# Optimization experiments

Measured on AMD Instinct MI355X. Metric: run time of the kernel, lower is better.

The kernel has to match this reference:

```python
import jax, jax.numpy as jnp
import numpy as np

D_MODEL = 1024
NUM_HEADS = 16
D_K = D_MODEL // NUM_HEADS


def setup_inputs() -> dict:
    key = jax.random.key(0)
    ks = jax.random.split(key, 11)
    B, S = 2, 2048
    scale = 1.0 / np.sqrt(D_MODEL)
    inp = {
        "q": jax.random.normal(ks[0], (B, S, D_MODEL), jnp.float32),
        "k": jax.random.normal(ks[1], (B, S, D_MODEL), jnp.float32),
        "v": jax.random.normal(ks[2], (B, S, D_MODEL), jnp.float32),
        "wq_w": jax.random.normal(ks[3], (D_MODEL, D_MODEL), jnp.float32) * scale,
        "wq_b": jnp.zeros((D_MODEL,), jnp.float32),
        "wk_w": jax.random.normal(ks[4], (D_MODEL, D_MODEL), jnp.float32) * scale,
        "wk_b": jnp.zeros((D_MODEL,), jnp.float32),
        "wv_w": jax.random.normal(ks[5], (D_MODEL, D_MODEL), jnp.float32) * scale,
        "wv_b": jnp.zeros((D_MODEL,), jnp.float32),
        "wo_w": jax.random.normal(ks[6], (D_MODEL, D_MODEL), jnp.float32) * scale,
        "wo_b": jnp.zeros((D_MODEL,), jnp.float32),
    }
    return inp


def reference(q, k, v, wq_w, wq_b, wk_w, wk_b, wv_w, wv_b, wo_w, wo_b):
    B, S, _ = q.shape
    H, dk = NUM_HEADS, D_K
    # projections (torch Linear: x @ W.T + b); reshape to [B, H, S, dk]
    qh = (q @ wq_w.T + wq_b).reshape(B, S, H, dk).transpose(0, 2, 1, 3)
    kh = (k @ wk_w.T + wk_b).reshape(B, S, H, dk).transpose(0, 2, 1, 3)
    vh = (v @ wv_w.T + wv_b).reshape(B, S, H, dk).transpose(0, 2, 1, 3)
    # explicit [B,H,S,S] scores, softmax over keys
    scores = jnp.einsum('bhqd,bhkd->bhqk', qh, kh) / np.sqrt(dk).astype(jnp.float32)
    weights = jax.nn.softmax(scores, axis=-1)
    out = jnp.einsum('bhqk,bhkd->bhqd', weights, vh)
    out = out.transpose(0, 2, 1, 3).reshape(B, S, H * dk)
    return out @ wo_w.T + wo_b
```

## Files before the change

### kernel.cpp

```cpp
#include <hip/hip_runtime.h>

#define B_  2
#define S_  2048
#define D_  1024
#define H_  16
#define DK_ 64

typedef __bf16 bf16;
typedef __bf16 bf16x8 __attribute__((ext_vector_type(8)));
typedef __bf16 bf16x4 __attribute__((ext_vector_type(4)));
typedef float  f32x4  __attribute__((ext_vector_type(4)));

#define GLD16(gptr, lptr) __builtin_amdgcn_global_load_lds( \
    (const __attribute__((address_space(1))) void*)(gptr),  \
    (__attribute__((address_space(3))) void*)(lptr), 16, 0, 0)

__global__ __launch_bounds__(256) void cast_all(
    const float* __restrict__ q, const float* __restrict__ k, const float* __restrict__ v,
    const float* __restrict__ wq, const float* __restrict__ wk, const float* __restrict__ wv,
    const float* __restrict__ wo,
    bf16* __restrict__ qb, bf16* __restrict__ kb, bf16* __restrict__ vb,
    bf16* __restrict__ wqb, bf16* __restrict__ wkb, bf16* __restrict__ wvb,
    bf16* __restrict__ wob) {
  int blk = blockIdx.x;
  const float* in; bf16* out; int base;
  if      (blk < 2048) { in = q;  out = qb;  base = blk; }
  else if (blk < 4096) { in = k;  out = kb;  base = blk - 2048; }
  else if (blk < 6144) { in = v;  out = vb;  base = blk - 4096; }
  else if (blk < 6656) { in = wq; out = wqb; base = blk - 6144; }
  else if (blk < 7168) { in = wk; out = wkb; base = blk - 6656; }
  else if (blk < 7680) { in = wv; out = wvb; base = blk - 7168; }
  else                 { in = wo; out = wob; base = blk - 7680; }
  int i = (base * 256 + threadIdx.x) * 8;
  float4 a = *(const float4*)(in + i);
  float4 b = *(const float4*)(in + i + 4);
  bf16x8 o;
  o[0] = (bf16)a.x; o[1] = (bf16)a.y; o[2] = (bf16)a.z; o[3] = (bf16)a.w;
  o[4] = (bf16)b.x; o[5] = (bf16)b.y; o[6] = (bf16)b.z; o[7] = (bf16)b.w;
  *(bf16x8*)(out + i) = o;
}

__global__ __launch_bounds__(256, 6) void gemm_qkv(
    const bf16* __restrict__ qb, const bf16* __restrict__ kb, const bf16* __restrict__ vb,
    const bf16* __restrict__ wq, const bf16* __restrict__ wk, const bf16* __restrict__ wv,
    const float* __restrict__ biq, const float* __restrict__ bik, const float* __restrict__ biv,
    bf16* __restrict__ Qh, bf16* __restrict__ Kh, bf16* __restrict__ Vt) {
  __shared__ bf16 As[128 * 32];
  __shared__ bf16 Bs[64 * 32];
  const int z = blockIdx.y;
  const bf16 *A, *Bm; const float* bias; bf16* Cout;
  int bx, by, N;
  if (z == 0)      { A = qb; Bm = wq; bias = biq; Cout = Qh; }
  else if (z == 1) { A = kb; Bm = wk; bias = bik; Cout = Kh; }
  else             { A = wv; Bm = vb; bias = biv; Cout = Vt; }
  if (z < 2) { by = blockIdx.x & 31; bx = blockIdx.x >> 5; N = D_; }
  else       { bx = blockIdx.x & 63; by = blockIdx.x >> 6; N = B_ * S_; }
  const int K = D_;

  const int tid  = threadIdx.x;
  const int wave = tid >> 6, lane = tid & 63;
  const int g = lane >> 4, r = lane & 15;
  const int m0 = by * 128, n0 = bx * 64;

  f32x4 acc[2][4] = {};
  const int srow = tid >> 2;
  const int sp   = tid & 3;

  for (int k0 = 0; k0 < K; k0 += 32) {
    __syncthreads();
#pragma unroll
    for (int rep = 0; rep < 2; rep++) {
      int row = rep * 64 + srow;
      int bb  = sp ^ ((row >> 1) & 3);
      GLD16(A + (size_t)(m0 + row) * K + k0 + bb * 8, As + (rep * 256 + wave * 64) * 8);
    }
    {
      int row = srow;
      int bb  = sp ^ ((row >> 1) & 3);
      GLD16(Bm + (size_t)(n0 + row) * K + k0 + bb * 8, Bs + (wave * 64) * 8);
    }
    __syncthreads();

    bf16x8 af[2], bfr[4];
#pragma unroll
    for (int i = 0; i < 2; i++) {
      int row = wave * 32 + i * 16 + r;
      af[i] = *(const bf16x8*)(As + row * 32 + (g ^ ((row >> 1) & 3)) * 8);
    }
#pragma unroll
    for (int j = 0; j < 4; j++) {
      int row = j * 16 + r;
      bfr[j] = *(const bf16x8*)(Bs + row * 32 + (g ^ ((row >> 1) & 3)) * 8);
    }
#pragma unroll
    for (int i = 0; i < 2; i++)
#pragma unroll
      for (int j = 0; j < 4; j++)
        acc[i][j] = __builtin_amdgcn_mfma_f32_16x16x32_bf16(af[i], bfr[j], acc[i][j], 0, 0, 0);
  }

  const float qscale = 0.18033688f;
#pragma unroll
  for (int i = 0; i < 2; i++) {
#pragma unroll
    for (int j = 0; j < 4; j++) {
#pragma unroll
      for (int t = 0; t < 4; t++) {
        int mrow = m0 + wave * 32 + i * 16 + g * 4 + t;
        int col  = n0 + j * 16 + r;
        float val = acc[i][j][t];
        if (z < 2) {
          val += bias[col];
          if (z == 0) val *= qscale;
          int bb2 = mrow >> 11, s = mrow & (S_ - 1);
          int hh = col >> 6, d = col & 63;
          Cout[(((size_t)(bb2 * H_ + hh)) * S_ + s) * 64 + d] = (bf16)val;
        } else {
          val += bias[mrow];
          Cout[(size_t)mrow * N + col] = (bf16)val;
        }
      }
    }
  }
}

__global__ __launch_bounds__(256) void gemm_out(const bf16* __restrict__ A,
                                                const bf16* __restrict__ Bm,
                                                const float* __restrict__ bias,
                                                float* __restrict__ Cout) {
  __shared__ bf16 As[128 * 32];
  __shared__ bf16 Bs[64 * 32];
  const int K = D_, N = D_;
  const int tid  = threadIdx.x;
  const int wave = tid >> 6, lane = tid & 63;
  const int g = lane >> 4, r = lane & 15;
  const int m0 = blockIdx.y * 128, n0 = blockIdx.x * 64;

  f32x4 acc[2][4] = {};
  const int srow = tid >> 2;
  const int sp   = tid & 3;

  for (int k0 = 0; k0 < K; k0 += 32) {
    __syncthreads();
#pragma unroll
    for (int rep = 0; rep < 2; rep++) {
      int row = rep * 64 + srow;
      int bb  = sp ^ ((row >> 1) & 3);
      GLD16(A + (size_t)(m0 + row) * K + k0 + bb * 8, As + (rep * 256 + wave * 64) * 8);
    }
    {
      int row = srow;
      int bb  = sp ^ ((row >> 1) & 3);
      GLD16(Bm + (size_t)(n0 + row) * K + k0 + bb * 8, Bs + (wave * 64) * 8);
    }
    __syncthreads();

    bf16x8 af[2], bfr[4];
#pragma unroll
    for (int i = 0; i < 2; i++) {
      int row = wave * 32 + i * 16 + r;
      af[i] = *(const bf16x8*)(As + row * 32 + (g ^ ((row >> 1) & 3)) * 8);
    }
#pragma unroll
    for (int j = 0; j < 4; j++) {
      int row = j * 16 + r;
      bfr[j] = *(const bf16x8*)(Bs + row * 32 + (g ^ ((row >> 1) & 3)) * 8);
    }
#pragma unroll
    for (int i = 0; i < 2; i++)
#pragma unroll
      for (int j = 0; j < 4; j++)
        acc[i][j] = __builtin_amdgcn_mfma_f32_16x16x32_bf16(af[i], bfr[j], acc[i][j], 0, 0, 0);
  }

#pragma unroll
  for (int i = 0; i < 2; i++)
#pragma unroll
    for (int j = 0; j < 4; j++)
#pragma unroll
      for (int t = 0; t < 4; t++) {
        int mrow = m0 + wave * 32 + i * 16 + g * 4 + t;
        int col  = n0 + j * 16 + r;
        Cout[(size_t)mrow * N + col] = acc[i][j][t] + bias[col];
      }
}

__global__ __launch_bounds__(256, 4) void flash_attn(const bf16* __restrict__ Qh,
                                                     const bf16* __restrict__ Kh,
                                                     const bf16* __restrict__ Vt,
                                                     bf16* __restrict__ Apart,
                                                     float* __restrict__ Lpart) {
  __shared__ bf16 Ks[64 * 64];
  __shared__ bf16 Vs[64 * 64];
  __shared__ bf16 Ps[128 * 40];

  const int tid  = threadIdx.x;
  const int wave = tid >> 6, lane = tid & 63;
  const int g = lane >> 4, r = lane & 15;

  int qt = blockIdx.x >> 6;
  int kh = blockIdx.x & 1;
  int bh = (blockIdx.x >> 1) & 31;
  int h = bh & (H_ - 1), b = bh >> 4;

  const bf16* Kbase = Kh + ((size_t)bh * S_ + kh * 1024) * DK_;
  const bf16* Vbase = Vt + (size_t)h * 64 * (B_ * S_) + (size_t)b * S_ + kh * 1024;

  bf16x8 bq[2][2];
#pragma unroll
  for (int sq = 0; sq < 2; sq++) {
    int qrow = qt * 128 + wave * 32 + sq * 16 + r;
    const bf16* qp = Qh + ((size_t)bh * S_ + qrow) * DK_;
#pragma unroll
    for (int kc = 0; kc < 2; kc++)
      bq[sq][kc] = *(const bf16x8*)(qp + kc * 32 + g * 8);
  }

  f32x4 acc_o[2][4] = {};
  float l_run[2] = {0.f, 0.f};

  const int srow = tid >> 3, spp = tid & 7;

  for (int j0 = 0; j0 < 1024 / 64; j0++) {
    __syncthreads();
#pragma unroll
    for (int rep = 0; rep < 2; rep++) {
      int rr = rep * 32 + srow;
      int bb = spp ^ (rr & 7);
      GLD16(Kbase + (size_t)(j0 * 64 + rr) * 64 + bb * 8, Ks + rep * 2048 + wave * 512);
      GLD16(Vbase + (size_t)rr * (B_ * S_) + j0 * 64 + bb * 8, Vs + rep * 2048 + wave * 512);
    }
    __syncthreads();

    bf16x8 ak[4][2];
#pragma unroll
    for (int ks = 0; ks < 4; ks++) {
      int kr = ks * 16 + r;
#pragma unroll
      for (int kc = 0; kc < 2; kc++)
        ak[ks][kc] = *(const bf16x8*)(Ks + kr * 64 + (((kc * 4 + g) ^ (kr & 7)) * 8));
    }
    f32x4 sacc[2][4] = {};
#pragma unroll
    for (int sq = 0; sq < 2; sq++)
#pragma unroll
      for (int ks = 0; ks < 4; ks++)
#pragma unroll
        for (int kc = 0; kc < 2; kc++)
          sacc[sq][ks] = __builtin_amdgcn_mfma_f32_16x16x32_bf16(ak[ks][kc], bq[sq][kc],
                                                                 sacc[sq][ks], 0, 0, 0);

#pragma unroll
    for (int c = 0; c < 2; c++) {
#pragma unroll
      for (int sq = 0; sq < 2; sq++) {
        int qrow = wave * 32 + sq * 16 + r;
        float rs = 0.f;
#pragma unroll
        for (int k2 = 0; k2 < 2; k2++) {
          int ks = c * 2 + k2;
          bf16x4 pk;
#pragma unroll
          for (int t = 0; t < 4; t++) {
            float pv = __builtin_amdgcn_exp2f(sacc[sq][ks][t]);
            rs += pv;
            pk[t] = (bf16)pv;
          }
          *(bf16x4*)(Ps + qrow * 40 + k2 * 16 + g * 4) = pk;
        }
        l_run[sq] += rs;
      }
      asm volatile("s_waitcnt lgkmcnt(0)" ::: "memory");

      bf16x8 bp[2];
#pragma unroll
      for (int sq = 0; sq < 2; sq++) {
        int qrow = wave * 32 + sq * 16 + r;
        bp[sq] = *(const bf16x8*)(Ps + qrow * 40 + g * 8);
      }
#pragma unroll
      for (int dsub = 0; dsub < 4; dsub++) {
        int dr = dsub * 16 + r;
        bf16x8 av = *(const bf16x8*)(Vs + dr * 64 + (((c * 4 + g) ^ (dr & 7)) * 8));
#pragma unroll
        for (int sq = 0; sq < 2; sq++)
          acc_o[sq][dsub] = __builtin_amdgcn_mfma_f32_16x16x32_bf16(av, bp[sq],
                                                                    acc_o[sq][dsub], 0, 0, 0);
      }
    }
  }

#pragma unroll
  for (int sq = 0; sq < 2; sq++) {
    float l = l_run[sq];
    l += __shfl_xor(l, 16, 64);
    l += __shfl_xor(l, 32, 64);
    int s = qt * 128 + wave * 32 + sq * 16 + r;
    if (g == 0)
      Lpart[(size_t)kh * (B_ * H_ * S_) + (size_t)bh * S_ + s] = l;
    size_t base = (size_t)kh * (B_ * S_ * (size_t)D_) + ((size_t)b * S_ + s) * D_ + (size_t)h * 64;
#pragma unroll
    for (int dsub = 0; dsub < 4; dsub++) {
      bf16x4 o;
#pragma unroll
      for (int t = 0; t < 4; t++) o[t] = (bf16)(acc_o[sq][dsub][t]);
      *(bf16x4*)(Apart + base + dsub * 16 + g * 4) = o;
    }
  }
}

__global__ __launch_bounds__(256) void combine(const bf16* __restrict__ Apart,
                                               const float* __restrict__ Lpart,
                                               bf16* __restrict__ AO) {
  const size_t EQ = (size_t)B_ * S_ * D_;
  const int LHALF = B_ * H_ * S_;
  int idx = (blockIdx.x * 256 + threadIdx.x) * 8;
  int token = idx >> 10;
  int dcol  = idx & (D_ - 1);
  int b = token >> 11, s = token & (S_ - 1);
  int h = dcol >> 6;
  int li = (b * H_ + h) * S_ + s;
  float inv = 1.0f / (Lpart[li] + Lpart[li + LHALF]);
  bf16x8 a0 = *(const bf16x8*)(Apart + idx);
  bf16x8 a1 = *(const bf16x8*)(Apart + EQ + idx);
  bf16x8 o;
#pragma unroll
  for (int t = 0; t < 8; t++) o[t] = (bf16)(((float)a0[t] + (float)a1[t]) * inv);
  *(bf16x8*)(AO + idx) = o;
}

extern "C" void kernel_launch(void* const* d_in, const int* in_sizes, int n_in,
                              void* d_out, int out_size, void* d_ws, size_t ws_size,
                              hipStream_t stream) {
  const float* q    = (const float*)d_in[0];
  const float* k    = (const float*)d_in[1];
  const float* v    = (const float*)d_in[2];
  const float* wq_w = (const float*)d_in[3];
  const float* wq_b = (const float*)d_in[4];
  const float* wk_w = (const float*)d_in[5];
  const float* wk_b = (const float*)d_in[6];
  const float* wv_w = (const float*)d_in[7];
  const float* wv_b = (const float*)d_in[8];
  const float* wo_w = (const float*)d_in[9];
  const float* wo_b = (const float*)d_in[10];

  bf16* W = (bf16*)d_ws;
  const size_t NTOK = (size_t)B_ * S_;
  const size_t EQ = NTOK * D_;
  const size_t EW = (size_t)D_ * D_;
  bf16* qb  = W;
  bf16* kb  = qb  + EQ;
  bf16* vb  = kb  + EQ;
  bf16* Qhb = vb  + EQ;
  bf16* Khb = Qhb + EQ;
  bf16* Vtb = Khb + EQ;
  bf16* AOb = Vtb + EQ;
  bf16* wqb = AOb + EQ;
  bf16* wkb = wqb + EW;
  bf16* wvb = wkb + EW;
  bf16* wob = wvb + EW;

  bf16*  Apart = qb;
  float* Lpart = (float*)vb;

  cast_all<<<8192, 256, 0, stream>>>(q, k, v, wq_w, wk_w, wv_w, wo_w,
                                     qb, kb, vb, wqb, wkb, wvb, wob);

  gemm_qkv<<<dim3(512, 3), 256, 0, stream>>>(qb, kb, vb, wqb, wkb, wvb,
                                             wq_b, wk_b, wv_b, Qhb, Khb, Vtb);

  flash_attn<<<1024, 256, 0, stream>>>(Qhb, Khb, Vtb, Apart, Lpart);

  combine<<<2048, 256, 0, stream>>>(Apart, Lpart, AOb);

  gemm_out<<<dim3(D_ / 64, NTOK / 128), 256, 0, stream>>>(AOb, wob, wo_b, (float*)d_out);
}
```

Measured before the change: 229.4 us.

## Fuse fp32-to-bf16 casts into GEMM loads and combine step into output GEMM

Drops the standalone cast kernel. The QKV and output GEMMs now stream fp32 inputs and weights straight into LDS with a new swizzle and convert them to bf16 when building MFMA fragments. The split-K attention combine (sum the two partials, multiply by the inverse softmax denominator) moves into the output GEMM's A-fragment load, which removes the combine kernel and its intermediate buffer round trip. In exchange, the GEMMs now read fp32 data, which doubles global and LDS traffic per tile and uses more LDS per block. Each fragment load also does extra conversion ALU work, and the output GEMM reads two A partial tiles.

Measured after the change: 281.0 us. 1.22x slower.

```diff
diff --git a/kernel.cpp b/kernel.cpp
--- a/kernel.cpp
+++ b/kernel.cpp
@@ -15,44 +15,19 @@
     (const __attribute__((address_space(1))) void*)(gptr),  \
     (__attribute__((address_space(3))) void*)(lptr), 16, 0, 0)
 
-__global__ __launch_bounds__(256) void cast_all(
-    const float* __restrict__ q, const float* __restrict__ k, const float* __restrict__ v,
-    const float* __restrict__ wq, const float* __restrict__ wk, const float* __restrict__ wv,
-    const float* __restrict__ wo,
-    bf16* __restrict__ qb, bf16* __restrict__ kb, bf16* __restrict__ vb,
-    bf16* __restrict__ wqb, bf16* __restrict__ wkb, bf16* __restrict__ wvb,
-    bf16* __restrict__ wob) {
-  int blk = blockIdx.x;
-  const float* in; bf16* out; int base;
-  if      (blk < 2048) { in = q;  out = qb;  base = blk; }
-  else if (blk < 4096) { in = k;  out = kb;  base = blk - 2048; }
-  else if (blk < 6144) { in = v;  out = vb;  base = blk - 4096; }
-  else if (blk < 6656) { in = wq; out = wqb; base = blk - 6144; }
-  else if (blk < 7168) { in = wk; out = wkb; base = blk - 6656; }
-  else if (blk < 7680) { in = wv; out = wvb; base = blk - 7168; }
-  else                 { in = wo; out = wob; base = blk - 7680; }
-  int i = (base * 256 + threadIdx.x) * 8;
-  float4 a = *(const float4*)(in + i);
-  float4 b = *(const float4*)(in + i + 4);
-  bf16x8 o;
-  o[0] = (bf16)a.x; o[1] = (bf16)a.y; o[2] = (bf16)a.z; o[3] = (bf16)a.w;
-  o[4] = (bf16)b.x; o[5] = (bf16)b.y; o[6] = (bf16)b.z; o[7] = (bf16)b.w;
-  *(bf16x8*)(out + i) = o;
-}
-
 __global__ __launch_bounds__(256, 6) void gemm_qkv(
-    const bf16* __restrict__ qb, const bf16* __restrict__ kb, const bf16* __restrict__ vb,
-    const bf16* __restrict__ wq, const bf16* __restrict__ wk, const bf16* __restrict__ wv,
+    const float* __restrict__ qf, const float* __restrict__ kf, const float* __restrict__ vf,
+    const float* __restrict__ wqf, const float* __restrict__ wkf, const float* __restrict__ wvf,
     const float* __restrict__ biq, const float* __restrict__ bik, const float* __restrict__ biv,
     bf16* __restrict__ Qh, bf16* __restrict__ Kh, bf16* __restrict__ Vt) {
-  __shared__ bf16 As[128 * 32];
-  __shared__ bf16 Bs[64 * 32];
+  __shared__ float Asf[128 * 32];
+  __shared__ float Bsf[64 * 32];
   const int z = blockIdx.y;
-  const bf16 *A, *Bm; const float* bias; bf16* Cout;
+  const float *A, *Bm, *bias; bf16* Cout;
   int bx, by, N;
-  if (z == 0)      { A = qb; Bm = wq; bias = biq; Cout = Qh; }
-  else if (z == 1) { A = kb; Bm = wk; bias = bik; Cout = Kh; }
-  else             { A = wv; Bm = vb; bias = biv; Cout = Vt; }
+  if (z == 0)      { A = qf;  Bm = wqf; bias = biq; Cout = Qh; }
+  else if (z == 1) { A = kf;  Bm = wkf; bias = bik; Cout = Kh; }
+  else             { A = wvf; Bm = vf;  bias = biv; Cout = Vt; }
   if (z < 2) { by = blockIdx.x & 31; bx = blockIdx.x >> 5; N = D_; }
   else       { bx = blockIdx.x & 63; by = blockIdx.x >> 6; N = B_ * S_; }
   const int K = D_;
@@ -63,21 +38,26 @@
   const int m0 = by * 128, n0 = bx * 64;
 
   f32x4 acc[2][4] = {};
-  const int srow = tid >> 2;
-  const int sp   = tid & 3;
+  const int srow = tid >> 3;
+  const int p    = tid & 7;
 
   for (int k0 = 0; k0 < K; k0 += 32) {
     __syncthreads();
 #pragma unroll
+    for (int rep = 0; rep < 4; rep++) {
+      int row = rep * 32 + srow;
+      int sb = (p >> 1) ^ (row & 3);
+      int hf = (p & 1) ^ ((row >> 2) & 1);
+      GLD16(A + (size_t)(m0 + row) * K + k0 + sb * 8 + hf * 4,
+            Asf + (rep * 32 + wave * 8) * 32);
+    }
+#pragma unroll
     for (int rep = 0; rep < 2; rep++) {
-      int row = rep * 64 + srow;
-      int bb  = sp ^ ((row >> 1) & 3);
-      GLD16(A + (size_t)(m0 + row) * K + k0 + bb * 8, As + (rep * 256 + wave * 64) * 8);
-    }
-    {
-      int row = srow;
-      int bb  = sp ^ ((row >> 1) & 3);
-      GLD16(Bm + (size_t)(n0 + row) * K + k0 + bb * 8, Bs + (wave * 64) * 8);
+      int row = rep * 32 + srow;
+      int sb = (p >> 1) ^ (row & 3);
+      int hf = (p & 1) ^ ((row >> 2) & 1);
+      GLD16(Bm + (size_t)(n0 + row) * K + k0 + sb * 8 + hf * 4,
+            Bsf + (rep * 32 + wave * 8) * 32);
     }
     __syncthreads();
 
@@ -85,12 +65,24 @@
 #pragma unroll
     for (int i = 0; i < 2; i++) {
       int row = wave * 32 + i * 16 + r;
-      af[i] = *(const bf16x8*)(As + row * 32 + (g ^ ((row >> 1) & 3)) * 8);
+      int s = g ^ (row & 3), h0 = (row >> 2) & 1;
+      float4 lo = *(const float4*)(Asf + row * 32 + (s * 2 + h0) * 4);
+      float4 hi = *(const float4*)(Asf + row * 32 + (s * 2 + (h0 ^ 1)) * 4);
+      bf16x8 o;
+      o[0]=(bf16)lo.x; o[1]=(bf16)lo.y; o[2]=(bf16)lo.z; o[3]=(bf16)lo.w;
+      o[4]=(bf16)hi.x; o[5]=(bf16)hi.y; o[6]=(bf16)hi.z; o[7]=(bf16)hi.w;
+      af[i] = o;
     }
 #pragma unroll
     for (int j = 0; j < 4; j++) {
       int row = j * 16 + r;
-      bfr[j] = *(const bf16x8*)(Bs + row * 32 + (g ^ ((row >> 1) & 3)) * 8);
+      int s = g ^ (row & 3), h0 = (row >> 2) & 1;
+      float4 lo = *(const float4*)(Bsf + row * 32 + (s * 2 + h0) * 4);
+      float4 hi = *(const float4*)(Bsf + row * 32 + (s * 2 + (h0 ^ 1)) * 4);
+      bf16x8 o;
+      o[0]=(bf16)lo.x; o[1]=(bf16)lo.y; o[2]=(bf16)lo.z; o[3]=(bf16)lo.w;
+      o[4]=(bf16)hi.x; o[5]=(bf16)hi.y; o[6]=(bf16)hi.z; o[7]=(bf16)hi.w;
+      bfr[j] = o;
     }
 #pragma unroll
     for (int i = 0; i < 2; i++)
@@ -124,67 +116,6 @@
   }
 }
 
-__global__ __launch_bounds__(256) void gemm_out(const bf16* __restrict__ A,
-                                                const bf16* __restrict__ Bm,
-                                                const float* __restrict__ bias,
-                                                float* __restrict__ Cout) {
-  __shared__ bf16 As[128 * 32];
-  __shared__ bf16 Bs[64 * 32];
-  const int K = D_, N = D_;
-  const int tid  = threadIdx.x;
-  const int wave = tid >> 6, lane = tid & 63;
-  const int g = lane >> 4, r = lane & 15;
-  const int m0 = blockIdx.y * 128, n0 = blockIdx.x * 64;
-
-  f32x4 acc[2][4] = {};
-  const int srow = tid >> 2;
-  const int sp   = tid & 3;
-
-  for (int k0 = 0; k0 < K; k0 += 32) {
-    __syncthreads();
-#pragma unroll
-    for (int rep = 0; rep < 2; rep++) {
-      int row = rep * 64 + srow;
-      int bb  = sp ^ ((row >> 1) & 3);
-      GLD16(A + (size_t)(m0 + row) * K + k0 + bb * 8, As + (rep * 256 + wave * 64) * 8);
-    }
-    {
-      int row = srow;
-      int bb  = sp ^ ((row >> 1) & 3);
-      GLD16(Bm + (size_t)(n0 + row) * K + k0 + bb * 8, Bs + (wave * 64) * 8);
-    }
-    __syncthreads();
-
-    bf16x8 af[2], bfr[4];
-#pragma unroll
-    for (int i = 0; i < 2; i++) {
-      int row = wave * 32 + i * 16 + r;
-      af[i] = *(const bf16x8*)(As + row * 32 + (g ^ ((row >> 1) & 3)) * 8);
-    }
-#pragma unroll
-    for (int j = 0; j < 4; j++) {
-      int row = j * 16 + r;
-      bfr[j] = *(const bf16x8*)(Bs + row * 32 + (g ^ ((row >> 1) & 3)) * 8);
-    }
-#pragma unroll
-    for (int i = 0; i < 2; i++)
-#pragma unroll
-      for (int j = 0; j < 4; j++)
-        acc[i][j] = __builtin_amdgcn_mfma_f32_16x16x32_bf16(af[i], bfr[j], acc[i][j], 0, 0, 0);
-  }
-
-#pragma unroll
-  for (int i = 0; i < 2; i++)
-#pragma unroll
-    for (int j = 0; j < 4; j++)
-#pragma unroll
-      for (int t = 0; t < 4; t++) {
-        int mrow = m0 + wave * 32 + i * 16 + g * 4 + t;
-        int col  = n0 + j * 16 + r;
-        Cout[(size_t)mrow * N + col] = acc[i][j][t] + bias[col];
-      }
-}
-
 __global__ __launch_bounds__(256, 4) void flash_attn(const bf16* __restrict__ Qh,
                                                      const bf16* __restrict__ Kh,
                                                      const bf16* __restrict__ Vt,
@@ -309,24 +240,95 @@
   }
 }
 
-__global__ __launch_bounds__(256) void combine(const bf16* __restrict__ Apart,
-                                               const float* __restrict__ Lpart,
-                                               bf16* __restrict__ AO) {
-  const size_t EQ = (size_t)B_ * S_ * D_;
+__global__ __launch_bounds__(256) void gemm_out(const bf16* __restrict__ A0,
+                                                const bf16* __restrict__ A1,
+                                                const float* __restrict__ Wo,
+                                                const float* __restrict__ Lpart,
+                                                const float* __restrict__ bias,
+                                                float* __restrict__ Cout) {
+  __shared__ bf16  As0[128 * 32];
+  __shared__ bf16  As1[128 * 32];
+  __shared__ float Bsf[64 * 32];
+  __shared__ float invl[128 * 16];
+  const int K = D_, N = D_;
+  const int tid  = threadIdx.x;
+  const int wave = tid >> 6, lane = tid & 63;
+  const int g = lane >> 4, r = lane & 15;
+  const int by = blockIdx.x & 31, bx = blockIdx.x >> 5;
+  const int m0 = by * 128, n0 = bx * 64;
   const int LHALF = B_ * H_ * S_;
-  int idx = (blockIdx.x * 256 + threadIdx.x) * 8;
-  int token = idx >> 10;
-  int dcol  = idx & (D_ - 1);
-  int b = token >> 11, s = token & (S_ - 1);
-  int h = dcol >> 6;
-  int li = (b * H_ + h) * S_ + s;
-  float inv = 1.0f / (Lpart[li] + Lpart[li + LHALF]);
-  bf16x8 a0 = *(const bf16x8*)(Apart + idx);
-  bf16x8 a1 = *(const bf16x8*)(Apart + EQ + idx);
-  bf16x8 o;
-#pragma unroll
-  for (int t = 0; t < 8; t++) o[t] = (bf16)(((float)a0[t] + (float)a1[t]) * inv);
-  *(bf16x8*)(AO + idx) = o;
+
+  for (int e = tid; e < 128 * 16; e += 256) {
+    int row = e >> 4, hh = e & 15;
+    int m = m0 + row;
+    int li = ((m >> 11) * H_ + hh) * S_ + (m & (S_ - 1));
+    invl[e] = 1.0f / (Lpart[li] + Lpart[li + LHALF]);
+  }
+
+  f32x4 acc[2][4] = {};
+  const int srowA = tid >> 2, spA = tid & 3;
+  const int srowB = tid >> 3, pB  = tid & 7;
+
+  for (int k0 = 0; k0 < K; k0 += 32) {
+    __syncthreads();
+#pragma unroll
+    for (int rep = 0; rep < 2; rep++) {
+      int row = rep * 64 + srowA;
+      int bb  = spA ^ ((row >> 1) & 3);
+      GLD16(A0 + (size_t)(m0 + row) * K + k0 + bb * 8, As0 + (rep * 256 + wave * 64) * 8);
+      GLD16(A1 + (size_t)(m0 + row) * K + k0 + bb * 8, As1 + (rep * 256 + wave * 64) * 8);
+    }
+#pragma unroll
+    for (int rep = 0; rep < 2; rep++) {
+      int row = rep * 32 + srowB;
+      int sb = (pB >> 1) ^ (row & 3);
+      int hf = (pB & 1) ^ ((row >> 2) & 1);
+      GLD16(Wo + (size_t)(n0 + row) * K + k0 + sb * 8 + hf * 4,
+            Bsf + (rep * 32 + wave * 8) * 32);
+    }
+    __syncthreads();
+
+    const int head = k0 >> 6;
+    bf16x8 af[2], bfr[4];
+#pragma unroll
+    for (int i = 0; i < 2; i++) {
+      int row = wave * 32 + i * 16 + r;
+      bf16x8 a0 = *(const bf16x8*)(As0 + row * 32 + (g ^ ((row >> 1) & 3)) * 8);
+      bf16x8 a1 = *(const bf16x8*)(As1 + row * 32 + (g ^ ((row >> 1) & 3)) * 8);
+      float sc = invl[row * 16 + head];
+      bf16x8 o;
+#pragma unroll
+      for (int t = 0; t < 8; t++) o[t] = (bf16)(((float)a0[t] + (float)a1[t]) * sc);
+      af[i] = o;
+    }
+#pragma unroll
+    for (int j = 0; j < 4; j++) {
+      int row = j * 16 + r;
+      int s = g ^ (row & 3), h0 = (row >> 2) & 1;
+      float4 lo = *(const float4*)(Bsf + row * 32 + (s * 2 + h0) * 4);
+      float4 hi = *(const float4*)(Bsf + row * 32 + (s * 2 + (h0 ^ 1)) * 4);
+      bf16x8 o;
+      o[0]=(bf16)lo.x; o[1]=(bf16)lo.y; o[2]=(bf16)lo.z; o[3]=(bf16)lo.w;
+      o[4]=(bf16)hi.x; o[5]=(bf16)hi.y; o[6]=(bf16)hi.z; o[7]=(bf16)hi.w;
+      bfr[j] = o;
+    }
+#pragma unroll
+    for (int i = 0; i < 2; i++)
+#pragma unroll
+      for (int j = 0; j < 4; j++)
+        acc[i][j] = __builtin_amdgcn_mfma_f32_16x16x32_bf16(af[i], bfr[j], acc[i][j], 0, 0, 0);
+  }
+
+#pragma unroll
+  for (int i = 0; i < 2; i++)
+#pragma unroll
+    for (int j = 0; j < 4; j++)
+#pragma unroll
+      for (int t = 0; t < 4; t++) {
+        int mrow = m0 + wave * 32 + i * 16 + g * 4 + t;
+        int col  = n0 + j * 16 + r;
+        Cout[(size_t)mrow * N + col] = acc[i][j][t] + bias[col];
+      }
 }
 
 extern "C" void kernel_launch(void* const* d_in, const int* in_sizes, int n_in,
@@ -347,31 +349,16 @@
   bf16* W = (bf16*)d_ws;
   const size_t NTOK = (size_t)B_ * S_;
   const size_t EQ = NTOK * D_;
-  const size_t EW = (size_t)D_ * D_;
-  bf16* qb  = W;
-  bf16* kb  = qb  + EQ;
-  bf16* vb  = kb  + EQ;
-  bf16* Qhb = vb  + EQ;
-  bf16* Khb = Qhb + EQ;
-  bf16* Vtb = Khb + EQ;
-  bf16* AOb = Vtb + EQ;
-  bf16* wqb = AOb + EQ;
-  bf16* wkb = wqb + EW;
-  bf16* wvb = wkb + EW;
-  bf16* wob = wvb + EW;
-
-  bf16*  Apart = qb;
-  float* Lpart = (float*)vb;
-
-  cast_all<<<8192, 256, 0, stream>>>(q, k, v, wq_w, wk_w, wv_w, wo_w,
-                                     qb, kb, vb, wqb, wkb, wvb, wob);
-
-  gemm_qkv<<<dim3(512, 3), 256, 0, stream>>>(qb, kb, vb, wqb, wkb, wvb,
+  bf16* Qhb   = W;
+  bf16* Khb   = Qhb + EQ;
+  bf16* Vtb   = Khb + EQ;
+  bf16* Apart = Vtb + EQ;
+  float* Lpart = (float*)(Apart + 2 * EQ);
+
+  gemm_qkv<<<dim3(512, 3), 256, 0, stream>>>(q, k, v, wq_w, wk_w, wv_w,
                                              wq_b, wk_b, wv_b, Qhb, Khb, Vtb);
 
   flash_attn<<<1024, 256, 0, stream>>>(Qhb, Khb, Vtb, Apart, Lpart);
 
-  combine<<<2048, 256, 0, stream>>>(Apart, Lpart, AOb);
-
-  gemm_out<<<dim3(D_ / 64, NTOK / 128), 256, 0, stream>>>(AOb, wob, wo_b, (float*)d_out);
+  gemm_out<<<512, 256, 0, stream>>>(Apart, Apart + EQ, wo_w, Lpart, wo_b, (float*)d_out);
 }
```
